# Optimization experiments

Measured on AMD Instinct MI355X. Metric: run time of the kernel, lower is better.

## Reference

```python
import jax, jax.numpy as jnp
import numpy as np

B, L, C, H = 4, 1024, 768, 12
D = C // H  # head_ch = 64


def setup_inputs() -> dict:
    key = jax.random.key(0)
    ks = jax.random.split(key, 8)
    s = 1.0 / np.sqrt(C)
    return {
        "inputs_q": jax.random.normal(ks[0], (B, L, C), jnp.float32),
        "inputs_kv": jax.random.normal(ks[1], (B, L, C), jnp.float32),
        "Wq": jax.random.normal(ks[2], (C, H * D), jnp.float32) * s,
        "Wk": jax.random.normal(ks[3], (C, H * D), jnp.float32) * s,
        "Wv": jax.random.normal(ks[4], (C, H * D), jnp.float32) * s,
        "Wout": jax.random.normal(ks[5], (H * D, C), jnp.float32) * s,
        "W_pre": jax.random.normal(ks[6], (H, H), jnp.float32) * (1.0 / np.sqrt(H)),
        "W_post": jax.random.normal(ks[7], (H, H), jnp.float32) * (1.0 / np.sqrt(H)),
    }


def reference(inputs_q, inputs_kv, Wq, Wk, Wv, Wout, W_pre, W_post):
    # Linear projections (no bias), split into heads: b l (h d) -> b h l d
    def split_heads(x):
        b, l, _ = x.shape
        return x.reshape(b, l, H, D).transpose(0, 2, 1, 3)

    q = split_heads(inputs_q @ Wq) / jnp.sqrt(jnp.asarray(D, inputs_q.dtype))
    k = split_heads(inputs_kv @ Wk)
    v = split_heads(inputs_kv @ Wv)

    # Attention logits [b, h, l, k]
    weights = jnp.einsum('bhld,bhkd->bhlk', q, k)
    # Talking-heads: learned cross-head mixing pre-softmax
    weights = jnp.einsum('bhlk,hi->bilk', weights, W_pre)
    weights = jax.nn.softmax(weights, axis=-1)
    # Talking-heads post-softmax mixing
    weights = jnp.einsum('bhlk,hi->bilk', weights, W_post)

    scores = jnp.einsum('bhlk,bhkd->bhld', weights, v)
    scores = scores.transpose(0, 2, 1, 3).reshape(B, L, H * D)  # b l (h d)
    return scores @ Wout
```

## Files before the change

### kernel.cpp

```cpp
#include <hip/hip_runtime.h>
#include <hip/hip_bf16.h>

#define BB 4
#define LL 1024
#define CC 768
#define HH 12
#define DD 64

typedef unsigned short ushort_t;
typedef __attribute__((ext_vector_type(8))) short bf16x8;
typedef __attribute__((ext_vector_type(4))) float f32x4;
typedef __attribute__((ext_vector_type(2))) float f32x2;
typedef __attribute__((ext_vector_type(2))) unsigned u32x2;

__device__ inline ushort_t f2bf(float x) {
    union { float f; unsigned u; } v; v.f = x;
    unsigned r = (v.u + 0x7FFFu + ((v.u >> 16) & 1u)) >> 16;
    return (ushort_t)r;
}
__device__ inline float u2f(unsigned u) {
    union { unsigned u; float f; } v; v.u = u;
    return v.f;
}
__device__ inline unsigned pack2bf(float lo, float hi) {
    union { __hip_bfloat162 v; unsigned u; } r;
    r.v = __float22bfloat162_rn(make_float2(lo, hi));
    return r.u;
}

__device__ inline void stage_rows(const ushort_t* __restrict__ g, int stride,
                                  ushort_t* lds, int nbytes, int wave, int lane) {
    const int ko = (lane & 3) << 3;
    const int rsub = lane >> 2;
    for (int off = wave * 1024; off < nbytes; off += 4096) {
        int row = (off >> 6) + rsub;
        __builtin_amdgcn_global_load_lds(
            (const __attribute__((address_space(1))) void*)(g + (size_t)row * stride + ko),
            (__attribute__((address_space(3))) void*)(lds + (off >> 1)),
            16, 0, 0);
    }
}

__global__ __launch_bounds__(256) void prep(const float* __restrict__ q, const float* __restrict__ kv,
                                            const float* __restrict__ w0, const float* __restrict__ w1,
                                            const float* __restrict__ w2, const float* __restrict__ w3,
                                            ushort_t* __restrict__ qo, ushort_t* __restrict__ kvo,
                                            ushort_t* __restrict__ o0, ushort_t* __restrict__ o1,
                                            ushort_t* __restrict__ o2, ushort_t* __restrict__ o3,
                                            float* __restrict__ Zp) {
    __shared__ float t[32][33];
    const int bx = blockIdx.x;
    if (bx < 3072) {
        const float* src = bx < 1536 ? q : kv;
        ushort_t* dst = bx < 1536 ? qo : kvo;
        int bb = bx < 1536 ? bx : bx - 1536;
        size_t i = ((size_t)bb * 256 + threadIdx.x) * 8;
        float4 a = *(const float4*)(src + i);
        float4 b = *(const float4*)(src + i + 4);
        ushort_t u[8] = {f2bf(a.x), f2bf(a.y), f2bf(a.z), f2bf(a.w),
                         f2bf(b.x), f2bf(b.y), f2bf(b.z), f2bf(b.w)};
        *(uint4*)(dst + i) = *(uint4*)u;
    } else if (bx < 5376) {
        int w = bx - 3072;
        int z = w / 576, rem = w % 576;
        const float* W = z == 0 ? w0 : z == 1 ? w1 : z == 2 ? w2 : w3;
        ushort_t* Wt   = z == 0 ? o0 : z == 1 ? o1 : z == 2 ? o2 : o3;
        const int c = threadIdx.x & 31, r0 = threadIdx.x >> 5;
        const int kb = (rem / 24) * 32, nb = (rem % 24) * 32;
#pragma unroll
        for (int i = 0; i < 4; ++i)
            t[r0 + 8 * i][c] = W[(size_t)(kb + r0 + 8 * i) * CC + nb + c];
        __syncthreads();
#pragma unroll
        for (int i = 0; i < 4; ++i)
            Wt[(size_t)(nb + r0 + 8 * i) * CC + kb + c] = f2bf(t[c][r0 + 8 * i]);
    } else {
        Zp[(bx - 5376) * 256 + threadIdx.x] = 0.f;
    }
}

__global__ __launch_bounds__(256) void proj_gemm(const ushort_t* __restrict__ Aq,
                                                 const ushort_t* __restrict__ Akv,
                                                 const ushort_t* __restrict__ Wqt,
                                                 const ushort_t* __restrict__ Wkt,
                                                 const ushort_t* __restrict__ Wvt,
                                                 ushort_t* __restrict__ Qo,
                                                 ushort_t* __restrict__ Ko,
                                                 ushort_t* __restrict__ Vto) {
    const int z = blockIdx.z;
    const ushort_t* A  = (z == 0) ? Aq : Akv;
    const ushort_t* Wt = (z == 0) ? Wqt : (z == 1 ? Wkt : Wvt);

    __shared__ __align__(16) ushort_t a_lds[128 * 32];
    __shared__ __align__(16) ushort_t b_lds[128 * 32];

    const int tid = threadIdx.x;
    const int bm = blockIdx.x * 128, bn = blockIdx.y * 128;
    const int wave = tid >> 6, lane = tid & 63;
    const int quad = lane >> 4, lq = lane & 15;
    const int wr = wave >> 1, wc = wave & 1;

    f32x4 acc[4][4] = {};

    for (int k0 = 0; k0 < CC; k0 += 32) {
        stage_rows(A + (size_t)bm * CC + k0, CC, a_lds, 8192, wave, lane);
        stage_rows(Wt + (size_t)bn * CC + k0, CC, b_lds, 8192, wave, lane);
        __syncthreads();
        bf16x8 af[4], bfr[4];
#pragma unroll
        for (int mi = 0; mi < 4; ++mi)
            af[mi] = *(bf16x8*)&a_lds[(wr * 64 + mi * 16 + lq) * 32 + quad * 8];
#pragma unroll
        for (int ni = 0; ni < 4; ++ni)
            bfr[ni] = *(bf16x8*)&b_lds[(wc * 64 + ni * 16 + lq) * 32 + quad * 8];
#pragma unroll
        for (int mi = 0; mi < 4; ++mi)
#pragma unroll
            for (int ni = 0; ni < 4; ++ni)
                acc[mi][ni] = __builtin_amdgcn_mfma_f32_16x16x32_bf16(af[mi], bfr[ni], acc[mi][ni], 0, 0, 0);
        __syncthreads();
    }

    const float scale = (z == 0) ? 0.125f : 1.0f;
#pragma unroll
    for (int mi = 0; mi < 4; ++mi)
#pragma unroll
        for (int ni = 0; ni < 4; ++ni)
#pragma unroll
            for (int r = 0; r < 4; ++r) {
                int row = bm + wr * 64 + mi * 16 + quad * 4 + r;
                int col = bn + wc * 64 + ni * 16 + lq;
                int b = row >> 10, l = row & 1023, h = col >> 6, d = col & 63;
                ushort_t v = f2bf(acc[mi][ni][r] * scale);
                if (z == 2) {
                    Vto[((size_t)(b * HH + h) * DD + d) * LL + l] = v;
                } else {
                    size_t off = (size_t)(b * HH + h) * (LL * DD)
                               + (size_t)(((l >> 4) * 8 + (d >> 3)) * 128 + (l & 15) * 8 + (d & 7));
                    if (z == 0) Qo[off] = v;
                    else        Ko[off] = v;
                }
            }
}

__global__ __launch_bounds__(256) void qk_premix(const ushort_t* __restrict__ Qf,
                                                 const ushort_t* __restrict__ Kf,
                                                 const float* __restrict__ Wpre,
                                                 ushort_t* __restrict__ E,
                                                 float* __restrict__ Z) {
    const int tid = threadIdx.x;
    const int lane = tid & 63, wave = tid >> 6;
    const int quad = lane >> 4, lq = lane & 15;
    const int wr = wave >> 1, wc = wave & 1;

    const int x = blockIdx.x;
    const int xcd = x & 7;
    const int b = xcd >> 1;
    const int s = x >> 3;
    const int bk = (s & 31) << 5;
    const int bl = ((((s >> 5) << 1) | (xcd & 1))) << 5;

    const ushort_t* Kp = Kf + (size_t)b * HH * LL * DD
                       + (size_t)(((bk >> 4) + wr) * 1024 + quad * 128 + lq * 8);
    const ushort_t* Qp = Qf + (size_t)b * HH * LL * DD
                       + (size_t)(((bl >> 4) + wc) * 1024 + quad * 128 + lq * 8);

    f32x4 acc[HH] = {};
#pragma unroll
    for (int h = 0; h < HH; ++h) {
        const size_t ho = (size_t)h * (LL * DD);
        bf16x8 ka0 = *(const bf16x8*)(Kp + ho);
        bf16x8 ka1 = *(const bf16x8*)(Kp + ho + 512);
        bf16x8 qb0 = *(const bf16x8*)(Qp + ho);
        bf16x8 qb1 = *(const bf16x8*)(Qp + ho + 512);
        acc[h] = __builtin_amdgcn_mfma_f32_16x16x32_bf16(ka0, qb0, acc[h], 0, 0, 0);
        acc[h] = __builtin_amdgcn_mfma_f32_16x16x32_bf16(ka1, qb1, acc[h], 0, 0, 0);
    }

    unsigned pk[6][4];
#pragma unroll
    for (int i2 = 0; i2 < 6; ++i2) {
        f32x4 m0 = {}, m1 = {};
#pragma unroll
        for (int h = 0; h < HH; ++h) {
            m0 += acc[h] * Wpre[h * HH + 2 * i2];
            m1 += acc[h] * Wpre[h * HH + 2 * i2 + 1];
        }
#pragma unroll
        for (int r = 0; r < 4; ++r)
            pk[i2][r] = pack2bf(__expf(m0[r]), __expf(m1[r]));
    }

    float zp[HH];
#pragma unroll
    for (int i2 = 0; i2 < 6; ++i2) {
        float s0 = 0.f, s1 = 0.f;
#pragma unroll
        for (int r = 0; r < 4; ++r) {
            s0 += u2f(pk[i2][r] << 16);
            s1 += u2f(pk[i2][r] & 0xFFFF0000u);
        }
        zp[2 * i2] = s0; zp[2 * i2 + 1] = s1;
    }
#pragma unroll
    for (int i = 0; i < HH; ++i) {
        zp[i] += __shfl_xor(zp[i], 16);
        zp[i] += __shfl_xor(zp[i], 32);
    }
    if (quad == 0) {
#pragma unroll
        for (int i = 0; i < HH; ++i)
            atomicAdd(&Z[((size_t)b * HH + i) * LL + bl + wc * 16 + lq], zp[i]);
    }

#pragma unroll
    for (int r = 0; r < 4; ++r) {
        ushort_t* ep = E + (((size_t)b * LL + bk + wr * 16 + quad * 4 + r) * LL
                            + bl + wc * 16 + lq) * HH;
        u32x2 s0; s0.x = pk[0][r]; s0.y = pk[1][r];
        u32x2 s1; s1.x = pk[2][r]; s1.y = pk[3][r];
        u32x2 s2; s2.x = pk[4][r]; s2.y = pk[5][r];
        __builtin_nontemporal_store(s0, (u32x2*)ep);
        __builtin_nontemporal_store(s1, (u32x2*)(ep + 4));
        __builtin_nontemporal_store(s2, (u32x2*)(ep + 8));
    }
}

__global__ __launch_bounds__(256, 3) void pv_postmix(const ushort_t* __restrict__ E,
                                                     const ushort_t* __restrict__ Vt,
                                                     const float* __restrict__ Wpost,
                                                     const float* __restrict__ Z,
                                                     ushort_t* __restrict__ att) {
    __shared__ __align__(16) ushort_t p_lds[2][6 * 16 * 64];

    const int tid = threadIdx.x;
    const int lane = tid & 63, wave = tid >> 6;
    const int quad = lane >> 4, lq = lane & 15;
    const int wd = wave;
    const int lmix = tid & 15, kp = tid >> 4;

    const int bid = blockIdx.x;
    const int xcd = bid & 7;
    const int b = xcd >> 1;
    const int s = bid >> 3;
    const int hg = s >> 5;
    const int ig = hg * 6;
    const int bl = ((((s & 31) << 1) | (xcd & 1))) << 4;

    float invZ[HH];
#pragma unroll
    for (int h = 0; h < HH; ++h)
        invZ[h] = 1.0f / Z[((size_t)b * HH + h) * LL + bl + lmix];

    const size_t estep = (size_t)LL * HH;
    const ushort_t* ebase = E + (((size_t)b * LL + kp * 4) * LL + bl + lmix) * HH;
    const size_t vbase = ((size_t)(b * HH + ig) * DD + wd * 16 + lq) * LL;

    f32x4 acc[6] = {};
    u32x2 er[12];

#pragma unroll
    for (int u = 0; u < 2; ++u)
#pragma unroll
        for (int j = 0; j < 3; ++j) {
            er[u * 6 + j]     = *(const u32x2*)(ebase + (size_t)(2 * u) * estep + 4 * j);
            er[u * 6 + 3 + j] = *(const u32x2*)(ebase + (size_t)(2 * u + 1) * estep + 4 * j);
        }

#pragma unroll 1
    for (int kt = 0; kt < 16; ++kt) {
        unsigned pkw[2][6];
#pragma unroll
        for (int u = 0; u < 2; ++u) {
            unsigned w0[6] = {er[u*6+0].x, er[u*6+0].y, er[u*6+1].x, er[u*6+1].y, er[u*6+2].x, er[u*6+2].y};
            unsigned w1[6] = {er[u*6+3].x, er[u*6+3].y, er[u*6+4].x, er[u*6+4].y, er[u*6+5].x, er[u*6+5].y};
            f32x2 m[6] = {};
#pragma unroll
            for (int h2 = 0; h2 < 6; ++h2) {
                f32x2 pe, po;
                pe.x = u2f(w0[h2] << 16);           pe.y = u2f(w1[h2] << 16);
                po.x = u2f(w0[h2] & 0xFFFF0000u);   po.y = u2f(w1[h2] & 0xFFFF0000u);
                pe *= invZ[2 * h2];
                po *= invZ[2 * h2 + 1];
#pragma unroll
                for (int i = 0; i < 6; ++i) {
                    m[i] += pe * Wpost[(2 * h2) * HH + ig + i];
                    m[i] += po * Wpost[(2 * h2 + 1) * HH + ig + i];
                }
            }
#pragma unroll
            for (int i = 0; i < 6; ++i) pkw[u][i] = pack2bf(m[i].x, m[i].y);
        }

        if (kt < 15) {
            const ushort_t* ep = ebase + (size_t)(kt + 1) * 64 * estep;
#pragma unroll
            for (int u = 0; u < 2; ++u)
#pragma unroll
                for (int j = 0; j < 3; ++j) {
                    er[u * 6 + j]     = *(const u32x2*)(ep + (size_t)(2 * u) * estep + 4 * j);
                    er[u * 6 + 3 + j] = *(const u32x2*)(ep + (size_t)(2 * u + 1) * estep + 4 * j);
                }
        }

        {
            unsigned* pw = (unsigned*)p_lds[kt & 1];
#pragma unroll
            for (int u = 0; u < 2; ++u) {
                const int w = kp * 2 + u;
                const int word = (((w >> 2) ^ (lmix & 7)) << 2) + (w & 3);
#pragma unroll
                for (int i = 0; i < 6; ++i)
                    pw[(i * 16 + lmix) * 32 + word] = pkw[u][i];
            }
        }

        asm volatile("s_waitcnt lgkmcnt(0)" ::: "memory");
        __builtin_amdgcn_s_barrier();
        asm volatile("" ::: "memory");

        const ushort_t* pb = p_lds[kt & 1];
#pragma unroll
        for (int k0 = 0; k0 < 2; ++k0) {
            bf16x8 vf[6];
#pragma unroll
            for (int ii = 0; ii < 6; ++ii)
                vf[ii] = *(const bf16x8*)(Vt + vbase + (size_t)ii * (DD * LL)
                                          + kt * 64 + k0 * 32 + quad * 8);
            const int chs = ((k0 << 2) + quad) ^ (lq & 7);
#pragma unroll
            for (int ii = 0; ii < 6; ++ii) {
                bf16x8 pa = *(bf16x8*)&pb[(ii * 16 + lq) * 64 + chs * 8];
                acc[ii] = __builtin_amdgcn_mfma_f32_16x16x32_bf16(pa, vf[ii], acc[ii], 0, 0, 0);
            }
        }
    }

#pragma unroll
    for (int ii = 0; ii < 6; ++ii)
#pragma unroll
        for (int r = 0; r < 4; ++r)
            att[((size_t)b * LL + bl + quad * 4 + r) * CC + (ig + ii) * 64 + wd * 16 + lq] =
                f2bf(acc[ii][r]);
}

__global__ __launch_bounds__(256) void out_gemm(const ushort_t* __restrict__ A,
                                                const ushort_t* __restrict__ Wt,
                                                float* __restrict__ out) {
    __shared__ __align__(16) ushort_t a_lds[128 * 32];
    __shared__ __align__(16) ushort_t b_lds[64 * 32];

    const int tid = threadIdx.x;
    const int bm = blockIdx.x * 128, bn = blockIdx.y * 64;
    const int wave = tid >> 6, lane = tid & 63;
    const int quad = lane >> 4, lq = lane & 15;
    const int wr = wave >> 1, wc = wave & 1;

    f32x4 acc[4][2] = {};

    for (int k0 = 0; k0 < CC; k0 += 32) {
        stage_rows(A + (size_t)bm * CC + k0, CC, a_lds, 8192, wave, lane);
        stage_rows(Wt + (size_t)bn * CC + k0, CC, b_lds, 4096, wave, lane);
        __syncthreads();
        bf16x8 af[4], bfr[2];
#pragma unroll
        for (int mi = 0; mi < 4; ++mi)
            af[mi] = *(bf16x8*)&a_lds[(wr * 64 + mi * 16 + lq) * 32 + quad * 8];
#pragma unroll
        for (int ni = 0; ni < 2; ++ni)
            bfr[ni] = *(bf16x8*)&b_lds[(wc * 32 + ni * 16 + lq) * 32 + quad * 8];
#pragma unroll
        for (int mi = 0; mi < 4; ++mi)
#pragma unroll
            for (int ni = 0; ni < 2; ++ni)
                acc[mi][ni] = __builtin_amdgcn_mfma_f32_16x16x32_bf16(af[mi], bfr[ni], acc[mi][ni], 0, 0, 0);
        __syncthreads();
    }

#pragma unroll
    for (int mi = 0; mi < 4; ++mi)
#pragma unroll
        for (int ni = 0; ni < 2; ++ni)
#pragma unroll
            for (int r = 0; r < 4; ++r) {
                int row = bm + wr * 64 + mi * 16 + quad * 4 + r;
                int col = bn + wc * 32 + ni * 16 + lq;
                out[(size_t)row * CC + col] = acc[mi][ni][r];
            }
}

extern "C" void kernel_launch(void* const* d_in, const int* in_sizes, int n_in,
                              void* d_out, int out_size, void* d_ws, size_t ws_size,
                              hipStream_t stream) {
    const float* inputs_q  = (const float*)d_in[0];
    const float* inputs_kv = (const float*)d_in[1];
    const float* Wq   = (const float*)d_in[2];
    const float* Wk   = (const float*)d_in[3];
    const float* Wv   = (const float*)d_in[4];
    const float* Wout = (const float*)d_in[5];
    const float* Wpre  = (const float*)d_in[6];
    const float* Wpost = (const float*)d_in[7];
    float* out = (float*)d_out;

    const size_t nS   = (size_t)BB * HH * LL * LL;
    const size_t nQKV = (size_t)BB * HH * LL * DD;
    const size_t nW   = (size_t)CC * CC;

    ushort_t* Eb   = (ushort_t*)d_ws;
    ushort_t* Qb   = Eb + nS;
    ushort_t* Kb   = Qb + nQKV;
    ushort_t* Vtb  = Kb + nQKV;
    ushort_t* attb = Vtb + nQKV;
    ushort_t* inq  = attb + nQKV;
    ushort_t* inkv = inq + nQKV;
    ushort_t* Wqt  = inkv + nQKV;
    ushort_t* Wkt  = Wqt + nW;
    ushort_t* Wvt  = Wkt + nW;
    ushort_t* Wot  = Wvt + nW;
    float*    Zb   = (float*)(Wot + nW);

    dim3 blk(256);

    prep<<<dim3(5568), blk, 0, stream>>>(inputs_q, inputs_kv, Wq, Wk, Wv, Wout,
                                         inq, inkv, Wqt, Wkt, Wvt, Wot, Zb);
    proj_gemm<<<dim3(32, 6, 3), blk, 0, stream>>>(inq, inkv, Wqt, Wkt, Wvt, Qb, Kb, Vtb);
    qk_premix<<<dim3(4096), blk, 0, stream>>>(Qb, Kb, Wpre, Eb, Zb);
    pv_postmix<<<dim3(512), blk, 0, stream>>>(Eb, Vtb, Wpost, Zb, attb);
    out_gemm<<<dim3(32, 12), blk, 0, stream>>>(attb, Wot, out);
}
```

Before: 264.6 us.

## Tile E layout per query tile and stage it into LDS via async global_load_lds

The producer kernel now writes the exp-logit tensor E in a layout blocked by 16-query tiles, so each pv_postmix block reads a contiguous slice. pv_postmix double-buffers that slice into LDS with global_load_lds and explicit vmcnt waits, and hoists all V fragment loads to the top of each iteration. The aim is to replace strided 8-byte global gathers with wide contiguous async copies overlapped with compute. In exchange LDS use grows and occupancy is lowered from 3 to 2 blocks per SM.

```diff
diff --git a/kernel.cpp b/kernel.cpp
--- a/kernel.cpp
+++ b/kernel.cpp
@@ -213,10 +213,11 @@
             atomicAdd(&Z[((size_t)b * HH + i) * LL + bl + wc * 16 + lq], zp[i]);
     }
 
+    const int ltw = (bl >> 4) + wc;
 #pragma unroll
     for (int r = 0; r < 4; ++r) {
-        ushort_t* ep = E + (((size_t)b * LL + bk + wr * 16 + quad * 4 + r) * LL
-                            + bl + wc * 16 + lq) * HH;
+        const int k = bk + wr * 16 + quad * 4 + r;
+        ushort_t* ep = E + (((size_t)(b * 64 + ltw) * 1024 + k) * 16 + lq) * 12;
         u32x2 s0; s0.x = pk[0][r]; s0.y = pk[1][r];
         u32x2 s1; s1.x = pk[2][r]; s1.y = pk[3][r];
         u32x2 s2; s2.x = pk[4][r]; s2.y = pk[5][r];
@@ -226,11 +227,12 @@
     }
 }
 
-__global__ __launch_bounds__(256, 3) void pv_postmix(const ushort_t* __restrict__ E,
+__global__ __launch_bounds__(256, 2) void pv_postmix(const ushort_t* __restrict__ E,
                                                      const ushort_t* __restrict__ Vt,
                                                      const float* __restrict__ Wpost,
                                                      const float* __restrict__ Z,
                                                      ushort_t* __restrict__ att) {
+    __shared__ __align__(16) ushort_t e_lds[2][64 * 16 * 12];
     __shared__ __align__(16) ushort_t p_lds[2][6 * 16 * 64];
 
     const int tid = threadIdx.x;
@@ -245,35 +247,64 @@
     const int s = bid >> 3;
     const int hg = s >> 5;
     const int ig = hg * 6;
-    const int bl = ((((s & 31) << 1) | (xcd & 1))) << 4;
+    const int lt = ((s & 31) << 1) | (xcd & 1);
+    const int bl = lt << 4;
 
     float invZ[HH];
 #pragma unroll
     for (int h = 0; h < HH; ++h)
         invZ[h] = 1.0f / Z[((size_t)b * HH + h) * LL + bl + lmix];
 
-    const size_t estep = (size_t)LL * HH;
-    const ushort_t* ebase = E + (((size_t)b * LL + kp * 4) * LL + bl + lmix) * HH;
+    const ushort_t* eslice = E + (size_t)(b * 64 + lt) * 1024 * 192;
     const size_t vbase = ((size_t)(b * HH + ig) * DD + wd * 16 + lq) * LL;
 
     f32x4 acc[6] = {};
-    u32x2 er[12];
-
-#pragma unroll
-    for (int u = 0; u < 2; ++u)
-#pragma unroll
-        for (int j = 0; j < 3; ++j) {
-            er[u * 6 + j]     = *(const u32x2*)(ebase + (size_t)(2 * u) * estep + 4 * j);
-            er[u * 6 + 3 + j] = *(const u32x2*)(ebase + (size_t)(2 * u + 1) * estep + 4 * j);
-        }
+
+#define ESTAGE(kt_, buf_)                                                                      \
+    do {                                                                                       \
+        const ushort_t* sb_ = eslice + (size_t)((kt_)*64 + wave * 16) * 192;                   \
+        ushort_t* db_ = &e_lds[buf_][wave * 3072];                                             \
+        _Pragma("unroll")                                                                      \
+        for (int j_ = 0; j_ < 6; ++j_)                                                         \
+            __builtin_amdgcn_global_load_lds(                                                  \
+                (const __attribute__((address_space(1))) void*)(sb_ + j_ * 512 + lane * 8),    \
+                (__attribute__((address_space(3))) void*)(db_ + j_ * 512 + lane * 8),          \
+                16, 0, 0);                                                                     \
+    } while (0)
+
+    ESTAGE(0, 0);
 
 #pragma unroll 1
     for (int kt = 0; kt < 16; ++kt) {
+        bf16x8 vf[12];
+#pragma unroll
+        for (int k0 = 0; k0 < 2; ++k0)
+#pragma unroll
+            for (int ii = 0; ii < 6; ++ii)
+                vf[k0 * 6 + ii] = *(const bf16x8*)(Vt + vbase + (size_t)ii * (DD * LL)
+                                                   + kt * 64 + k0 * 32 + quad * 8);
+
+        if (kt < 15) {
+            ESTAGE(kt + 1, (kt + 1) & 1);
+            asm volatile("s_waitcnt vmcnt(18)" ::: "memory");
+        } else {
+            asm volatile("s_waitcnt vmcnt(12)" ::: "memory");
+        }
+        __builtin_amdgcn_sched_barrier(0);
+
+        const ushort_t* eb = e_lds[kt & 1];
         unsigned pkw[2][6];
 #pragma unroll
         for (int u = 0; u < 2; ++u) {
-            unsigned w0[6] = {er[u*6+0].x, er[u*6+0].y, er[u*6+1].x, er[u*6+1].y, er[u*6+2].x, er[u*6+2].y};
-            unsigned w1[6] = {er[u*6+3].x, er[u*6+3].y, er[u*6+4].x, er[u*6+4].y, er[u*6+5].x, er[u*6+5].y};
+            const ushort_t* ebp = eb + ((kp * 4 + 2 * u) - wave * 16) * 192 + wave * 3072 + lmix * 12;
+            u32x2 e0 = *(const u32x2*)(ebp);
+            u32x2 e1 = *(const u32x2*)(ebp + 4);
+            u32x2 e2 = *(const u32x2*)(ebp + 8);
+            u32x2 o0 = *(const u32x2*)(ebp + 192);
+            u32x2 o1 = *(const u32x2*)(ebp + 196);
+            u32x2 o2 = *(const u32x2*)(ebp + 200);
+            unsigned w0[6] = {e0.x, e0.y, e1.x, e1.y, e2.x, e2.y};
+            unsigned w1[6] = {o0.x, o0.y, o1.x, o1.y, o2.x, o2.y};
             f32x2 m[6] = {};
 #pragma unroll
             for (int h2 = 0; h2 < 6; ++h2) {
@@ -292,17 +323,6 @@
             for (int i = 0; i < 6; ++i) pkw[u][i] = pack2bf(m[i].x, m[i].y);
         }
 
-        if (kt < 15) {
-            const ushort_t* ep = ebase + (size_t)(kt + 1) * 64 * estep;
-#pragma unroll
-            for (int u = 0; u < 2; ++u)
-#pragma unroll
-                for (int j = 0; j < 3; ++j) {
-                    er[u * 6 + j]     = *(const u32x2*)(ep + (size_t)(2 * u) * estep + 4 * j);
-                    er[u * 6 + 3 + j] = *(const u32x2*)(ep + (size_t)(2 * u + 1) * estep + 4 * j);
-                }
-        }
-
         {
             unsigned* pw = (unsigned*)p_lds[kt & 1];
 #pragma unroll
@@ -322,19 +342,15 @@
         const ushort_t* pb = p_lds[kt & 1];
 #pragma unroll
         for (int k0 = 0; k0 < 2; ++k0) {
-            bf16x8 vf[6];
-#pragma unroll
-            for (int ii = 0; ii < 6; ++ii)
-                vf[ii] = *(const bf16x8*)(Vt + vbase + (size_t)ii * (DD * LL)
-                                          + kt * 64 + k0 * 32 + quad * 8);
             const int chs = ((k0 << 2) + quad) ^ (lq & 7);
 #pragma unroll
             for (int ii = 0; ii < 6; ++ii) {
                 bf16x8 pa = *(bf16x8*)&pb[(ii * 16 + lq) * 64 + chs * 8];
-                acc[ii] = __builtin_amdgcn_mfma_f32_16x16x32_bf16(pa, vf[ii], acc[ii], 0, 0, 0);
+                acc[ii] = __builtin_amdgcn_mfma_f32_16x16x32_bf16(pa, vf[k0 * 6 + ii], acc[ii], 0, 0, 0);
             }
         }
     }
+#undef ESTAGE
 
 #pragma unroll
     for (int ii = 0; ii < 6; ++ii)
```

Result: faster. 250.6 us (-5.3%).
